# Optimization experiments

Hardware: AMD Instinct MI355X
Metric: run time of the kernel (lower is better)

The kernel has to match this reference:

```python
import jax, jax.numpy as jnp
import numpy as np

NS = 48          # scalar channel multiplicity ('48x0e' input irreps)
NV = 10          # vector multiplicity ('10x1o' output irreps)
N = 20000        # nodes
E = 100000       # edges
W_NUMEL = NS * NS + NS * NV  # e3nn FullyConnectedTensorProduct weight_numel = 2784
OUT_DIM = NS + 3 * NV        # '48x0e + 10x1o' -> 78


def setup_inputs() -> dict:
    key = jax.random.key(0)
    ks = jax.random.split(key, 8)
    node_attr = jax.random.normal(ks[0], (N, NS), dtype=jnp.float32)
    edge_index = jax.random.randint(ks[1], (2, E), 0, N, dtype=jnp.int32)
    edge_attr = jax.random.normal(ks[2], (E, NS), dtype=jnp.float32)
    edge_sh = jax.random.normal(ks[3], (E, 9), dtype=jnp.float32)  # sh lmax=2: 1+3+5
    fc1_w = jax.random.normal(ks[4], (3 * NS, 3 * NS), dtype=jnp.float32) / np.float32(np.sqrt(3 * NS))
    fc1_b = jnp.zeros((3 * NS,), dtype=jnp.float32)
    fc2_w = jax.random.normal(ks[5], (3 * NS, W_NUMEL), dtype=jnp.float32) / np.float32(np.sqrt(3 * NS))
    fc2_b = jnp.zeros((W_NUMEL,), dtype=jnp.float32)
    return {"node_attr": node_attr, "edge_index": edge_index, "edge_attr": edge_attr,
            "edge_sh": edge_sh, "fc1_w": fc1_w, "fc1_b": fc1_b, "fc2_w": fc2_w, "fc2_b": fc2_b}


def reference(node_attr, edge_index, edge_attr, edge_sh, fc1_w, fc1_b, fc2_w, fc2_b):
    src, dst = edge_index[0], edge_index[1]
    # edge features = [edge_attr, src scalars, dst scalars]  (n_edge_features = 3*ns)
    ea = jnp.concatenate([edge_attr, node_attr[src, :NS], node_attr[dst, :NS]], axis=-1)
    # edge MLP -> per-edge tensor-product weights (shared_weights=False)
    h = jax.nn.relu(ea @ fc1_w + fc1_b)
    w = h @ fc2_w + fc2_b                      # [E, W_NUMEL]
    w0 = w[:, :NS * NS].reshape(E, NS, NS)     # path 0e x 0e -> 0e
    w1 = w[:, NS * NS:].reshape(E, NS, NV)     # path 0e x 1o -> 1o
    x = node_attr[dst]                         # gathered scalar node features [E, NS]
    sh0 = edge_sh[:, :1]                       # l=0 component [E,1]
    sh1 = edge_sh[:, 1:4]                      # l=1 components [E,3]
    norm = np.float32(1.0 / np.sqrt(NS))       # path fan-in normalization (mul1*mul2 = NS*1)
    out0 = jnp.einsum('ei,eik->ek', x, w0) * sh0 * norm                # [E, NS]
    out1 = jnp.einsum('ek,em->ekm', jnp.einsum('ei,eik->ek', x, w1), sh1) * norm  # [E, NV, 3]
    tp = jnp.concatenate([out0, out1.reshape(E, NV * 3)], axis=-1)     # [E, OUT_DIM]
    # scatter-mean to source nodes (reduce='mean', dim_size=N)
    summed = jax.ops.segment_sum(tp, src, num_segments=N)
    counts = jax.ops.segment_sum(jnp.ones((E, 1), tp.dtype), src, num_segments=N)
    return summed / jnp.maximum(counts, 1.0)
```

## Files before the change

kernel.cpp:

```cpp
#include <hip/hip_runtime.h>
#include <hip/hip_bf16.h>

#define NS_    48
#define NV_    10
#define N_NODE 20000
#define N_EDGE 100000
#define HID    144
#define OUTC   58
#define ODIM   78
#define TILE   64
#define LDE    160
#define WNUM   2784

typedef __attribute__((ext_vector_type(8))) short bf8;
typedef __attribute__((ext_vector_type(4))) float f32x4;

__device__ __forceinline__ short f2bf(float x) {
  __hip_bfloat16 h = __float2bfloat16(x);
  union { __hip_bfloat16 b; short s; } u; u.b = h; return u.s;
}

__global__ void prep_fc1(const float* __restrict__ w, short* __restrict__ dst) {
  int idx = blockIdx.x * 256 + threadIdx.x;
  if (idx >= 9 * 5 * 512) return;
  int j = idx & 7, l = (idx >> 3) & 63, t = idx >> 9;
  int ks = t % 5, nt = t / 5;
  int k = ks * 32 + ((l >> 4) << 3) + j;
  int n = nt * 16 + (l & 15);
  dst[idx] = f2bf(k < HID ? w[k * HID + n] : 0.f);
}

__global__ void prep_g(const float* __restrict__ w, const float* __restrict__ b,
                       short* __restrict__ dst) {
  int idx = blockIdx.x * 256 + threadIdx.x;
  if (idx >= 48 * 4 * 5 * 512) return;
  int j = idx & 7, l = (idx >> 3) & 63, t = idx >> 9;
  int ks = t % 5, u = t / 5;
  int strip = u & 3, i = u >> 2;
  int k = ks * 32 + ((l >> 4) << 3) + j;
  int c = strip * 16 + (l & 15);
  float v = 0.f;
  if (c < OUTC) {
    if (k < HID)
      v = (c < NS_) ? w[k * WNUM + i * NS_ + c]
                    : w[k * WNUM + NS_ * NS_ + i * NV_ + (c - NS_)];
    else if (k == HID)
      v = (c < NS_) ? b[i * NS_ + c]
                    : b[NS_ * NS_ + i * NV_ + (c - NS_)];
  }
  dst[idx] = f2bf(v);
}

__global__ void k_hist(const int* __restrict__ eidx, int* __restrict__ cnt) {
  int e = blockIdx.x * 256 + threadIdx.x;
  if (e < N_EDGE) atomicAdd(&cnt[eidx[e]], 1);
}

__global__ void k_scan1(const int* __restrict__ cnt, int* __restrict__ locexc,
                        int* __restrict__ blksum) {
  __shared__ int sh[256];
  int g = blockIdx.x * 256 + threadIdx.x;
  int v = (g < N_NODE) ? cnt[g] : 0;
  sh[threadIdx.x] = v;
  __syncthreads();
  for (int d = 1; d < 256; d <<= 1) {
    int t = (threadIdx.x >= d) ? sh[threadIdx.x - d] : 0;
    __syncthreads();
    sh[threadIdx.x] += t;
    __syncthreads();
  }
  if (g < N_NODE) locexc[g] = sh[threadIdx.x] - v;
  if (threadIdx.x == 255) blksum[blockIdx.x] = sh[255];
}

__global__ void k_scan2(const int* __restrict__ blksum, int* __restrict__ blkoff) {
  __shared__ int sh[128];
  int t = threadIdx.x;
  int v = (t < 79) ? blksum[t] : 0;
  sh[t] = v;
  __syncthreads();
  for (int d = 1; d < 128; d <<= 1) {
    int x = (t >= d) ? sh[t - d] : 0;
    __syncthreads();
    sh[t] += x;
    __syncthreads();
  }
  if (t < 79) blkoff[t] = sh[t] - v;
}

__global__ void k_scatter(const int* __restrict__ eidx, const int* __restrict__ locexc,
                          const int* __restrict__ blkoff, int* __restrict__ cursor,
                          int* __restrict__ sortedE) {
  int e = blockIdx.x * 256 + threadIdx.x;
  if (e >= N_EDGE) return;
  int s = eidx[e];
  int base = blkoff[s >> 8] + locexc[s];
  int r = atomicAdd(&cursor[s], 1);
  sortedE[base + r] = e;
}

__global__ __launch_bounds__(256, 3) void fused_edge(
    const float* __restrict__ node_attr, const int* __restrict__ eidx,
    const float* __restrict__ edge_attr, const float* __restrict__ edge_sh,
    const float* __restrict__ fc1_b, const int* __restrict__ sortedE,
    const short* __restrict__ gfrag, const short* __restrict__ fc1frag,
    float* __restrict__ out)
{
  __shared__ short EA[TILE * LDE];
  __shared__ float xT[NS_ * TILE];
  __shared__ float shs[TILE * 4];
  __shared__ int   srcs[TILE];
  __shared__ int   runStart[TILE + 1], runSrc[TILE];
  __shared__ int   nRunsSh;

  const int tid  = threadIdx.x;
  const int lane = tid & 63;
  const int wv   = tid >> 6;
  const int base = blockIdx.x * TILE;

  for (int t = tid; t < TILE * 16; t += 256) {
    int r = t >> 4, c = t & 15;
    EA[r * LDE + HID + c] = 0;
  }

  {
    const int el = tid >> 2, part = tid & 3;
    const int gi = base + el;
    const bool ev = gi < N_EDGE;
    const int e  = ev ? sortedE[gi] : 0;
    const int es = ev ? eidx[e] : 0;
    const int ed = ev ? eidx[N_EDGE + e] : 0;
    if (part == 0) {
      srcs[el] = ev ? es : -1;
      #pragma unroll
      for (int c = 0; c < 4; ++c) shs[el * 4 + c] = ev ? edge_sh[(size_t)e * 9 + c] : 0.f;
    }
    const float4* pa = (const float4*)(edge_attr + (size_t)e * NS_);
    const float4* ps = (const float4*)(node_attr + (size_t)es * NS_);
    const float4* pd = (const float4*)(node_attr + (size_t)ed * NS_);
    const float4 z4 = make_float4(0.f, 0.f, 0.f, 0.f);
    #pragma unroll
    for (int q = 0; q < 3; ++q) {
      const int c0 = part * 12 + q * 4;
      float4 va = ev ? pa[part * 3 + q] : z4;
      float4 vs = ev ? ps[part * 3 + q] : z4;
      float4 vd = ev ? pd[part * 3 + q] : z4;
      EA[el * LDE + c0 + 0] = f2bf(va.x);
      EA[el * LDE + c0 + 1] = f2bf(va.y);
      EA[el * LDE + c0 + 2] = f2bf(va.z);
      EA[el * LDE + c0 + 3] = f2bf(va.w);
      EA[el * LDE + NS_ + c0 + 0] = f2bf(vs.x);
      EA[el * LDE + NS_ + c0 + 1] = f2bf(vs.y);
      EA[el * LDE + NS_ + c0 + 2] = f2bf(vs.z);
      EA[el * LDE + NS_ + c0 + 3] = f2bf(vs.w);
      EA[el * LDE + 2 * NS_ + c0 + 0] = f2bf(vd.x);
      EA[el * LDE + 2 * NS_ + c0 + 1] = f2bf(vd.y);
      EA[el * LDE + 2 * NS_ + c0 + 2] = f2bf(vd.z);
      EA[el * LDE + 2 * NS_ + c0 + 3] = f2bf(vd.w);
      xT[(c0 + 0) * TILE + el] = vd.x;
      xT[(c0 + 1) * TILE + el] = vd.y;
      xT[(c0 + 2) * TILE + el] = vd.z;
      xT[(c0 + 3) * TILE + el] = vd.w;
    }
  }
  __syncthreads();

  {
    const int mrow = lane & 15;
    const int koff = (lane >> 4) << 3;
    bf8 aF[5];
    #pragma unroll
    for (int ks = 0; ks < 5; ++ks)
      aF[ks] = *(const bf8*)&EA[(wv * 16 + mrow) * LDE + ks * 32 + koff];
    #pragma unroll
    for (int nt = 0; nt < 9; ++nt) {
      f32x4 acc = {0.f, 0.f, 0.f, 0.f};
      #pragma unroll
      for (int ks = 0; ks < 5; ++ks) {
        bf8 bF = *(const bf8*)&fc1frag[((nt * 5 + ks) * 64 + lane) * 8];
        acc = __builtin_amdgcn_mfma_f32_16x16x32_bf16(aF[ks], bF, acc, 0, 0, 0);
      }
      const int col = nt * 16 + mrow;
      const float bb = fc1_b[col];
      #pragma unroll
      for (int r = 0; r < 4; ++r) {
        float h = acc[r] + bb;
        h = h > 0.f ? h : 0.f;
        EA[(wv * 16 + ((lane >> 4) << 2) + r) * LDE + col] = f2bf(h);
      }
    }
    if (lane < 16) EA[(wv * 16 + lane) * LDE + HID] = (short)0x3F80;
  }
  __syncthreads();

  {
    const int mrow = lane & 15;
    const int koff = (lane >> 4) << 3;
    const int g0 = (lane >> 4) << 2;

    f32x4 oacc[4];
    #pragma unroll
    for (int mt = 0; mt < 4; ++mt) oacc[mt] = (f32x4){0.f, 0.f, 0.f, 0.f};

    bf8 aF[4][5];
    #pragma unroll
    for (int mt = 0; mt < 4; ++mt)
      #pragma unroll
      for (int ks = 0; ks < 5; ++ks) {
        aF[mt][ks] = *(const bf8*)&EA[(mt * 16 + mrow) * LDE + ks * 32 + koff];
        asm volatile("" : "+v"(aF[mt][ks]));
      }
    __syncthreads();

    const short* gb = gfrag + wv * 2560 + lane * 8;
    bf8 bA[5], bB[5];
    #pragma unroll
    for (int ks = 0; ks < 5; ++ks) bA[ks] = *(const bf8*)(gb + ks * 512);

    auto compute = [&](const bf8 (&BF)[5], int i) {
      #pragma unroll
      for (int mt = 0; mt < 4; ++mt) {
        f32x4 wi = {0.f, 0.f, 0.f, 0.f};
        #pragma unroll
        for (int ks = 0; ks < 5; ++ks)
          wi = __builtin_amdgcn_mfma_f32_16x16x32_bf16(aF[mt][ks], BF[ks], wi, 0, 0, 0);
        const float4 xs = *(const float4*)&xT[i * TILE + mt * 16 + g0];
        oacc[mt][0] += xs.x * wi[0];
        oacc[mt][1] += xs.y * wi[1];
        oacc[mt][2] += xs.z * wi[2];
        oacc[mt][3] += xs.w * wi[3];
      }
    };

    for (int i = 0; i < NS_; i += 2) {
      #pragma unroll
      for (int ks = 0; ks < 5; ++ks)
        bB[ks] = *(const bf8*)(gb + (i + 1) * 10240 + ks * 512);
      compute(bA, i);
      const int ip = (i + 2 < NS_) ? (i + 2) : (NS_ - 1);
      #pragma unroll
      for (int ks = 0; ks < 5; ++ks)
        bA[ks] = *(const bf8*)(gb + ip * 10240 + ks * 512);
      compute(bB, i + 1);
    }

    float* O = (float*)EA;
    const float nrm = 0.14433756729740643f;
    const int col = wv * 16 + mrow;
    #pragma unroll
    for (int mt = 0; mt < 4; ++mt) {
      #pragma unroll
      for (int r = 0; r < 4; ++r) {
        const int row = mt * 16 + g0 + r;
        const float v = oacc[mt][r] * nrm;
        if (col < NS_) {
          O[row * 80 + col] = v * shs[row * 4 + 0];
        } else if (col < OUTC) {
          const int kp = col - NS_;
          O[row * 80 + NS_ + kp * 3 + 0] = v * shs[row * 4 + 1];
          O[row * 80 + NS_ + kp * 3 + 1] = v * shs[row * 4 + 2];
          O[row * 80 + NS_ + kp * 3 + 2] = v * shs[row * 4 + 3];
        }
      }
    }
  }
  __syncthreads();

  if (tid < 64) {
    const int s = srcs[tid];
    const bool valid = s >= 0;
    const bool head = valid && (tid == 0 || srcs[tid - 1] != s);
    const unsigned long long hm = __ballot(head);
    const unsigned long long vm = __ballot(valid);
    const int rank = __popcll(hm & ((1ull << tid) - 1ull));
    if (head) { runStart[rank] = tid; runSrc[rank] = s; }
    if (tid == 0) {
      const int nR = __popcll(hm);
      nRunsSh = nR;
      runStart[nR] = __popcll(vm);
    }
  }
  __syncthreads();

  {
    const float* O = (const float*)EA;
    const int nR = nRunsSh;
    for (int t = tid; t < nR * ODIM; t += 256) {
      const int k = t / ODIM, c = t - k * ODIM;
      const int rs = runStart[k], re = runStart[k + 1];
      float s = 0.f;
      for (int r = rs; r < re; ++r) s += O[r * 80 + c];
      atomicAdd(&out[(size_t)runSrc[k] * ODIM + c], s);
    }
  }
}

__global__ void finalize(float* __restrict__ out, const int* __restrict__ cnt) {
  int idx = blockIdx.x * 256 + threadIdx.x;
  if (idx >= N_NODE * ODIM) return;
  int n = idx / ODIM;
  out[idx] = out[idx] / fmaxf((float)cnt[n], 1.f);
}

extern "C" void kernel_launch(void* const* d_in, const int* in_sizes, int n_in,
                              void* d_out, int out_size, void* d_ws, size_t ws_size,
                              hipStream_t stream) {
  (void)in_sizes; (void)n_in; (void)out_size; (void)ws_size;
  const float* node_attr = (const float*)d_in[0];
  const int*   eidx      = (const int*)d_in[1];
  const float* edge_attr = (const float*)d_in[2];
  const float* edge_sh   = (const float*)d_in[3];
  const float* fc1_w     = (const float*)d_in[4];
  const float* fc1_b     = (const float*)d_in[5];
  const float* fc2_w     = (const float*)d_in[6];
  const float* fc2_b     = (const float*)d_in[7];
  float* out = (float*)d_out;

  char* ws = (char*)d_ws;
  short* gfrag   = (short*)(ws);
  short* fc1frag = (short*)(ws + 983040);
  int*   cnt     = (int*)(ws + 1029120);
  int*   locexc  = (int*)(ws + 1109120);
  int*   cursor  = (int*)(ws + 1189120);
  int*   blksum  = (int*)(ws + 1269120);
  int*   blkoff  = (int*)(ws + 1269632);
  int*   sortedE = (int*)(ws + 1270144);

  hipMemsetAsync(out, 0, (size_t)N_NODE * ODIM * sizeof(float), stream);
  hipMemsetAsync(cnt, 0, N_NODE * sizeof(int), stream);
  hipMemsetAsync(cursor, 0, N_NODE * sizeof(int), stream);

  prep_fc1<<<(9 * 5 * 512 + 255) / 256, 256, 0, stream>>>(fc1_w, fc1frag);
  prep_g<<<(48 * 4 * 5 * 512 + 255) / 256, 256, 0, stream>>>(fc2_w, fc2_b, gfrag);

  k_hist<<<(N_EDGE + 255) / 256, 256, 0, stream>>>(eidx, cnt);
  k_scan1<<<(N_NODE + 255) / 256, 256, 0, stream>>>(cnt, locexc, blksum);
  k_scan2<<<1, 128, 0, stream>>>(blksum, blkoff);
  k_scatter<<<(N_EDGE + 255) / 256, 256, 0, stream>>>(eidx, locexc, blkoff, cursor, sortedE);

  fused_edge<<<(N_EDGE + TILE - 1) / TILE, 256, 0, stream>>>(
      node_attr, eidx, edge_attr, edge_sh, fc1_b, sortedE, gfrag, fc1frag, out);

  finalize<<<(N_NODE * ODIM + 255) / 256, 256, 0, stream>>>(out, cnt);
}
```

Measured before the change: 175.2 us.

## Double edge tile to 128 per block to reuse weight fragments

Doubles the edge tile from 64 to 128 edges per block, so each block loads the gfrag/fc1 B-fragments once for twice as many edges. The point is to cut the L2 traffic for the per-edge weight contraction. Staging, both MMA stages, the output write and the per-source run detection are adjusted to match, and run detection now combines ballot masks from two waves through shared memory. In exchange, register and LDS use roughly double and launch bounds drop to 2 blocks per CU, so the kernel risks spills, lower occupancy and a worse tail across the grid.

```diff
diff --git a/kernel.cpp b/kernel.cpp
--- a/kernel.cpp
+++ b/kernel.cpp
@@ -8,7 +8,7 @@
 #define HID    144
 #define OUTC   58
 #define ODIM   78
-#define TILE   64
+#define TILE   128
 #define LDE    160
 #define WNUM   2784
 
@@ -99,7 +99,7 @@
   sortedE[base + r] = e;
 }
 
-__global__ __launch_bounds__(256, 3) void fused_edge(
+__global__ __launch_bounds__(256, 2) void fused_edge(
     const float* __restrict__ node_attr, const int* __restrict__ eidx,
     const float* __restrict__ edge_attr, const float* __restrict__ edge_sh,
     const float* __restrict__ fc1_b, const int* __restrict__ sortedE,
@@ -111,6 +111,7 @@
   __shared__ float shs[TILE * 4];
   __shared__ int   srcs[TILE];
   __shared__ int   runStart[TILE + 1], runSrc[TILE];
+  __shared__ unsigned long long hmaskSh[2], vmaskSh[2];
   __shared__ int   nRunsSh;
 
   const int tid  = threadIdx.x;
@@ -124,7 +125,7 @@
   }
 
   {
-    const int el = tid >> 2, part = tid & 3;
+    const int el = tid >> 1, part = tid & 1;
     const int gi = base + el;
     const bool ev = gi < N_EDGE;
     const int e  = ev ? sortedE[gi] : 0;
@@ -140,11 +141,11 @@
     const float4* pd = (const float4*)(node_attr + (size_t)ed * NS_);
     const float4 z4 = make_float4(0.f, 0.f, 0.f, 0.f);
     #pragma unroll
-    for (int q = 0; q < 3; ++q) {
-      const int c0 = part * 12 + q * 4;
-      float4 va = ev ? pa[part * 3 + q] : z4;
-      float4 vs = ev ? ps[part * 3 + q] : z4;
-      float4 vd = ev ? pd[part * 3 + q] : z4;
+    for (int q = 0; q < 6; ++q) {
+      const int c0 = part * 24 + q * 4;
+      float4 va = ev ? pa[part * 6 + q] : z4;
+      float4 vs = ev ? ps[part * 6 + q] : z4;
+      float4 vd = ev ? pd[part * 6 + q] : z4;
       EA[el * LDE + c0 + 0] = f2bf(va.x);
       EA[el * LDE + c0 + 1] = f2bf(va.y);
       EA[el * LDE + c0 + 2] = f2bf(va.z);
@@ -168,28 +169,33 @@
   {
     const int mrow = lane & 15;
     const int koff = (lane >> 4) << 3;
-    bf8 aF[5];
-    #pragma unroll
-    for (int ks = 0; ks < 5; ++ks)
-      aF[ks] = *(const bf8*)&EA[(wv * 16 + mrow) * LDE + ks * 32 + koff];
+    bf8 aFf[2][5];
+    #pragma unroll
+    for (int mg = 0; mg < 2; ++mg)
+      #pragma unroll
+      for (int ks = 0; ks < 5; ++ks)
+        aFf[mg][ks] = *(const bf8*)&EA[(wv * 32 + mg * 16 + mrow) * LDE + ks * 32 + koff];
     #pragma unroll
     for (int nt = 0; nt < 9; ++nt) {
-      f32x4 acc = {0.f, 0.f, 0.f, 0.f};
+      f32x4 acc0 = {0.f, 0.f, 0.f, 0.f}, acc1 = {0.f, 0.f, 0.f, 0.f};
       #pragma unroll
       for (int ks = 0; ks < 5; ++ks) {
         bf8 bF = *(const bf8*)&fc1frag[((nt * 5 + ks) * 64 + lane) * 8];
-        acc = __builtin_amdgcn_mfma_f32_16x16x32_bf16(aF[ks], bF, acc, 0, 0, 0);
+        acc0 = __builtin_amdgcn_mfma_f32_16x16x32_bf16(aFf[0][ks], bF, acc0, 0, 0, 0);
+        acc1 = __builtin_amdgcn_mfma_f32_16x16x32_bf16(aFf[1][ks], bF, acc1, 0, 0, 0);
       }
       const int col = nt * 16 + mrow;
       const float bb = fc1_b[col];
+      const int rbase = wv * 32 + ((lane >> 4) << 2);
       #pragma unroll
       for (int r = 0; r < 4; ++r) {
-        float h = acc[r] + bb;
-        h = h > 0.f ? h : 0.f;
-        EA[(wv * 16 + ((lane >> 4) << 2) + r) * LDE + col] = f2bf(h);
-      }
-    }
-    if (lane < 16) EA[(wv * 16 + lane) * LDE + HID] = (short)0x3F80;
+        float h0 = acc0[r] + bb; h0 = h0 > 0.f ? h0 : 0.f;
+        float h1 = acc1[r] + bb; h1 = h1 > 0.f ? h1 : 0.f;
+        EA[(rbase + r) * LDE + col]      = f2bf(h0);
+        EA[(rbase + 16 + r) * LDE + col] = f2bf(h1);
+      }
+    }
+    if (lane < 32) EA[(wv * 32 + lane) * LDE + HID] = (short)0x3F80;
   }
   __syncthreads();
 
@@ -198,13 +204,13 @@
     const int koff = (lane >> 4) << 3;
     const int g0 = (lane >> 4) << 2;
 
-    f32x4 oacc[4];
-    #pragma unroll
-    for (int mt = 0; mt < 4; ++mt) oacc[mt] = (f32x4){0.f, 0.f, 0.f, 0.f};
-
-    bf8 aF[4][5];
-    #pragma unroll
-    for (int mt = 0; mt < 4; ++mt)
+    f32x4 oacc[8];
+    #pragma unroll
+    for (int mt = 0; mt < 8; ++mt) oacc[mt] = (f32x4){0.f, 0.f, 0.f, 0.f};
+
+    bf8 aF[8][5];
+    #pragma unroll
+    for (int mt = 0; mt < 8; ++mt)
       #pragma unroll
       for (int ks = 0; ks < 5; ++ks) {
         aF[mt][ks] = *(const bf8*)&EA[(mt * 16 + mrow) * LDE + ks * 32 + koff];
@@ -219,7 +225,7 @@
 
     auto compute = [&](const bf8 (&BF)[5], int i) {
       #pragma unroll
-      for (int mt = 0; mt < 4; ++mt) {
+      for (int mt = 0; mt < 8; ++mt) {
         f32x4 wi = {0.f, 0.f, 0.f, 0.f};
         #pragma unroll
         for (int ks = 0; ks < 5; ++ks)
@@ -248,7 +254,7 @@
     const float nrm = 0.14433756729740643f;
     const int col = wv * 16 + mrow;
     #pragma unroll
-    for (int mt = 0; mt < 4; ++mt) {
+    for (int mt = 0; mt < 8; ++mt) {
       #pragma unroll
       for (int r = 0; r < 4; ++r) {
         const int row = mt * 16 + g0 + r;
@@ -266,18 +272,27 @@
   }
   __syncthreads();
 
-  if (tid < 64) {
+  if (tid < TILE) {
     const int s = srcs[tid];
     const bool valid = s >= 0;
     const bool head = valid && (tid == 0 || srcs[tid - 1] != s);
     const unsigned long long hm = __ballot(head);
     const unsigned long long vm = __ballot(valid);
-    const int rank = __popcll(hm & ((1ull << tid) - 1ull));
+    if ((tid & 63) == 0) { hmaskSh[tid >> 6] = hm; vmaskSh[tid >> 6] = vm; }
+  }
+  __syncthreads();
+  if (tid < TILE) {
+    const int s = srcs[tid];
+    const bool valid = s >= 0;
+    const bool head = valid && (tid == 0 || srcs[tid - 1] != s);
+    const int w = tid >> 6, l = tid & 63;
+    const int rank = __popcll(hmaskSh[w] & ((1ull << l) - 1ull)) +
+                     (w ? __popcll(hmaskSh[0]) : 0);
     if (head) { runStart[rank] = tid; runSrc[rank] = s; }
     if (tid == 0) {
-      const int nR = __popcll(hm);
+      const int nR = __popcll(hmaskSh[0]) + __popcll(hmaskSh[1]);
       nRunsSh = nR;
-      runStart[nR] = __popcll(vm);
+      runStart[nR] = __popcll(vmaskSh[0]) + __popcll(vmaskSh[1]);
     }
   }
   __syncthreads();
```

After: 248.4 us. +41.8%, slower.

## Deepen weight-fragment prefetch to four buffers, pack bf16 stores, add setprio

Applied to the files above, without the earlier changes.

The per-i weight fragment loads in the fc2/tensor-product loop now use a four-deep register ring, three iterations ahead instead of one, to hide global load latency behind MFMA work. The compute section is wrapped in s_setprio to favour the MFMA wave. Edge-feature conversion now packs pairs of bf16 values into 64-bit LDS stores instead of scalar short stores. The occupancy hint in launch_bounds is dropped to make room for the extra registers, which may reduce waves per CU.

```diff
diff --git a/kernel.cpp b/kernel.cpp
--- a/kernel.cpp
+++ b/kernel.cpp
@@ -18,6 +18,9 @@
 __device__ __forceinline__ short f2bf(float x) {
   __hip_bfloat16 h = __float2bfloat16(x);
   union { __hip_bfloat16 b; short s; } u; u.b = h; return u.s;
+}
+__device__ __forceinline__ unsigned pk2(float a, float b) {
+  return (unsigned)(unsigned short)f2bf(a) | ((unsigned)(unsigned short)f2bf(b) << 16);
 }
 
 __global__ void prep_fc1(const float* __restrict__ w, short* __restrict__ dst) {
@@ -99,7 +102,7 @@
   sortedE[base + r] = e;
 }
 
-__global__ __launch_bounds__(256, 3) void fused_edge(
+__global__ __launch_bounds__(256) void fused_edge(
     const float* __restrict__ node_attr, const int* __restrict__ eidx,
     const float* __restrict__ edge_attr, const float* __restrict__ edge_sh,
     const float* __restrict__ fc1_b, const int* __restrict__ sortedE,
@@ -145,18 +148,9 @@
       float4 va = ev ? pa[part * 3 + q] : z4;
       float4 vs = ev ? ps[part * 3 + q] : z4;
       float4 vd = ev ? pd[part * 3 + q] : z4;
-      EA[el * LDE + c0 + 0] = f2bf(va.x);
-      EA[el * LDE + c0 + 1] = f2bf(va.y);
-      EA[el * LDE + c0 + 2] = f2bf(va.z);
-      EA[el * LDE + c0 + 3] = f2bf(va.w);
-      EA[el * LDE + NS_ + c0 + 0] = f2bf(vs.x);
-      EA[el * LDE + NS_ + c0 + 1] = f2bf(vs.y);
-      EA[el * LDE + NS_ + c0 + 2] = f2bf(vs.z);
-      EA[el * LDE + NS_ + c0 + 3] = f2bf(vs.w);
-      EA[el * LDE + 2 * NS_ + c0 + 0] = f2bf(vd.x);
-      EA[el * LDE + 2 * NS_ + c0 + 1] = f2bf(vd.y);
-      EA[el * LDE + 2 * NS_ + c0 + 2] = f2bf(vd.z);
-      EA[el * LDE + 2 * NS_ + c0 + 3] = f2bf(vd.w);
+      *(uint2*)&EA[el * LDE + c0]           = make_uint2(pk2(va.x, va.y), pk2(va.z, va.w));
+      *(uint2*)&EA[el * LDE + NS_ + c0]     = make_uint2(pk2(vs.x, vs.y), pk2(vs.z, vs.w));
+      *(uint2*)&EA[el * LDE + 2 * NS_ + c0] = make_uint2(pk2(vd.x, vd.y), pk2(vd.z, vd.w));
       xT[(c0 + 0) * TILE + el] = vd.x;
       xT[(c0 + 1) * TILE + el] = vd.y;
       xT[(c0 + 2) * TILE + el] = vd.z;
@@ -213,11 +207,15 @@
     __syncthreads();
 
     const short* gb = gfrag + wv * 2560 + lane * 8;
-    bf8 bA[5], bB[5];
-    #pragma unroll
-    for (int ks = 0; ks < 5; ++ks) bA[ks] = *(const bf8*)(gb + ks * 512);
+
+    auto loadB = [&](bf8 (&BF)[5], int i) {
+      const short* p = gb + i * 10240;
+      #pragma unroll
+      for (int ks = 0; ks < 5; ++ks) BF[ks] = *(const bf8*)(p + ks * 512);
+    };
 
     auto compute = [&](const bf8 (&BF)[5], int i) {
+      __builtin_amdgcn_s_setprio(1);
       #pragma unroll
       for (int mt = 0; mt < 4; ++mt) {
         f32x4 wi = {0.f, 0.f, 0.f, 0.f};
@@ -230,18 +228,20 @@
         oacc[mt][2] += xs.z * wi[2];
         oacc[mt][3] += xs.w * wi[3];
       }
+      __builtin_amdgcn_s_setprio(0);
     };
 
-    for (int i = 0; i < NS_; i += 2) {
-      #pragma unroll
-      for (int ks = 0; ks < 5; ++ks)
-        bB[ks] = *(const bf8*)(gb + (i + 1) * 10240 + ks * 512);
-      compute(bA, i);
-      const int ip = (i + 2 < NS_) ? (i + 2) : (NS_ - 1);
-      #pragma unroll
-      for (int ks = 0; ks < 5; ++ks)
-        bA[ks] = *(const bf8*)(gb + ip * 10240 + ks * 512);
-      compute(bB, i + 1);
+    bf8 b0[5], b1[5], b2[5], b3[5];
+    loadB(b0, 0); loadB(b1, 1); loadB(b2, 2);
+    for (int i = 0; i < NS_; i += 4) {
+      loadB(b3, i + 3);
+      compute(b0, i);
+      loadB(b0, (i + 4 < NS_) ? i + 4 : NS_ - 1);
+      compute(b1, i + 1);
+      loadB(b1, (i + 5 < NS_) ? i + 5 : NS_ - 1);
+      compute(b2, i + 2);
+      loadB(b2, (i + 6 < NS_) ? i + 6 : NS_ - 1);
+      compute(b3, i + 3);
     }
 
     float* O = (float*)EA;
```

Measured after the change: 225.2 us. 28.5% more time.
